# Kernel tuning notes

Hardware: AMD Instinct MI355X
Metric: run time of the kernel (lower is better)

The kernel has to match this reference:

```python
import jax, jax.numpy as jnp
import numpy as np
import math

VOCAB, D, H, L = 32000, 1024, 16, 4
HD = D // H
DFF = 4 * D
EPS = 1e-5


def setup_inputs() -> dict:
    key = jax.random.key(0)
    ks = jax.random.split(key, 20)
    B, T = 4, 1024
    s = 0.02
    inp = {
        'inputs': jax.random.randint(ks[0], (B, T), 0, VOCAB),
        'emb_table': jax.random.normal(ks[1], (VOCAB, D), jnp.float32) * s,
        'Wq': jax.random.normal(ks[2], (L, D, D), jnp.float32) * s,
        'bq': jnp.zeros((L, D), jnp.float32),
        'Wk': jax.random.normal(ks[3], (L, D, D), jnp.float32) * s,
        'bk': jnp.zeros((L, D), jnp.float32),
        'Wv': jax.random.normal(ks[4], (L, D, D), jnp.float32) * s,
        'bv': jnp.zeros((L, D), jnp.float32),
        'Wo': jax.random.normal(ks[5], (L, D, D), jnp.float32) * s,
        'bo': jnp.zeros((L, D), jnp.float32),
        'ln1_g': jnp.ones((L, D), jnp.float32),
        'ln1_b': jnp.zeros((L, D), jnp.float32),
        'W1': jax.random.normal(ks[6], (L, D, DFF), jnp.float32) * s,
        'b1': jnp.zeros((L, DFF), jnp.float32),
        'W2': jax.random.normal(ks[7], (L, DFF, D), jnp.float32) * s,
        'b2': jnp.zeros((L, D), jnp.float32),
        'ln2_g': jnp.ones((L, D), jnp.float32),
        'ln2_b': jnp.zeros((L, D), jnp.float32),
    }
    return inp


def _layernorm(x, g, b):
    mu = jnp.mean(x, axis=-1, keepdims=True)
    var = jnp.mean(jnp.square(x - mu), axis=-1, keepdims=True)
    return (x - mu) * jax.lax.rsqrt(var + EPS) * g + b


def _pos_emb(T):
    pos = jnp.arange(T, dtype=jnp.float32)[:, None]          # [T,1]
    div = jnp.exp(jnp.arange(0, D, 2, dtype=jnp.float32) * (-math.log(10000.0) / D))
    pe = jnp.zeros((T, D), jnp.float32)
    pe = pe.at[:, 0::2].set(jnp.sin(pos * div))
    pe = pe.at[:, 1::2].set(jnp.cos(pos * div))
    return pe


def reference(inputs, emb_table, Wq, bq, Wk, bk, Wv, bv, Wo, bo,
              ln1_g, ln1_b, W1, b1, W2, b2, ln2_g, ln2_b):
    B, T = inputs.shape
    x = emb_table[inputs] + _pos_emb(T)[None, :, :]          # [B,T,D]
    causal = jnp.tril(jnp.ones((T, T), bool))                # [T,T]
    scale = 1.0 / math.sqrt(HD)
    for l in range(L):
        q = (x @ Wq[l] + bq[l]).reshape(B, T, H, HD)
        k = (x @ Wk[l] + bk[l]).reshape(B, T, H, HD)
        v = (x @ Wv[l] + bv[l]).reshape(B, T, H, HD)
        scores = jnp.einsum('bqhd,bkhd->bhqk', q, k) * scale
        scores = jnp.where(causal, scores, -jnp.inf)
        w = jax.nn.softmax(scores, axis=-1)
        attn = jnp.einsum('bhqk,bkhd->bqhd', w, v).reshape(B, T, D)
        attn = attn @ Wo[l] + bo[l]
        x = _layernorm(x + attn, ln1_g[l], ln1_b[l])
        ff = jax.nn.relu(x @ W1[l] + b1[l]) @ W2[l] + b2[l]
        x = _layernorm(x + ff, ln2_g[l], ln2_b[l])
    return x
```

## Files before the change

### kernel.cpp

```cpp
#include <hip/hip_runtime.h>

typedef __attribute__((ext_vector_type(8))) __bf16 bf16x8;
typedef __attribute__((ext_vector_type(4))) float f32x4;
typedef __attribute__((ext_vector_type(8))) unsigned short ushort8;

#define DMODEL 1024
#define SEQ 1024
#define NLAYER 4

__device__ __forceinline__ unsigned short f2bf(float f) {
  unsigned u = __float_as_uint(f);
  u += 0x7fffu + ((u >> 16) & 1u);
  return (unsigned short)(u >> 16);
}

__device__ __forceinline__ float bf2f(unsigned short u) {
  return __uint_as_float((unsigned)u << 16);
}

__device__ __forceinline__ void async_copy16(const void* gsrc, const void* lds_dst) {
  __builtin_amdgcn_global_load_lds(
      (__attribute__((address_space(1))) void*)(unsigned long long)(gsrc),
      (__attribute__((address_space(3))) void*)(unsigned int)(unsigned long long)(lds_dst),
      16, 0, 0);
}

__device__ __forceinline__ f32x4 mfma16(bf16x8 a, bf16x8 b, f32x4 c) {
  return __builtin_amdgcn_mfma_f32_16x16x32_bf16(a, b, c, 0, 0, 0);
}

__global__ __launch_bounds__(256) void preproc_kernel(
    const int* __restrict__ tok, const float* __restrict__ emb,
    const float* __restrict__ Wq, const float* __restrict__ Wk,
    const float* __restrict__ Wv, const float* __restrict__ Wo,
    const float* __restrict__ W1, const float* __restrict__ W2,
    const float* __restrict__ bq, const float* __restrict__ bk,
    const float* __restrict__ bv,
    unsigned short* __restrict__ wqkv_t, unsigned short* __restrict__ wo_t,
    unsigned short* __restrict__ w1_t, unsigned short* __restrict__ w2_t,
    float* __restrict__ qkvb, unsigned short* __restrict__ xb) {
  __shared__ unsigned short tileT[64 * 136];
  const int bid = blockIdx.x;
  const int tid = threadIdx.x;
  if (bid < 6144) {
    const float* src; unsigned short* dst; size_t R, C; int tx, ty;
    if (bid < 2048) {
      int w = bid >> 9, z = (bid >> 7) & 3, tl = bid & 127;
      tx = tl & 15; ty = tl >> 4; R = 1024; C = 1024;
      if (w == 0)      { src = Wq + (size_t)z * 1048576; dst = wqkv_t + (size_t)z * 3145728; }
      else if (w == 1) { src = Wk + (size_t)z * 1048576; dst = wqkv_t + (size_t)z * 3145728 + 1048576; }
      else if (w == 2) { src = Wv + (size_t)z * 1048576; dst = wqkv_t + (size_t)z * 3145728 + 2097152; }
      else             { src = Wo + (size_t)z * 1048576; dst = wo_t + (size_t)z * 1048576; }
    } else if (bid < 4096) {
      int t = bid - 2048, z = t >> 9, tl = t & 511;
      tx = tl & 63; ty = tl >> 6; R = 1024; C = 4096;
      src = W1 + (size_t)z * 4194304; dst = w1_t + (size_t)z * 4194304;
    } else {
      int t = bid - 4096, z = t >> 9, tl = t & 511;
      tx = tl & 15; ty = tl >> 4; R = 4096; C = 1024;
      src = W2 + (size_t)z * 4194304; dst = w2_t + (size_t)z * 4194304;
    }
    const int c0 = tx * 64, r0 = ty * 128;
    const int s16 = tid & 15, hi = tid >> 4;
#pragma unroll
    for (int it = 0; it < 8; ++it) {
      const int r = it * 16 + hi;
      f32x4 v = __builtin_nontemporal_load(
          (const f32x4*)(src + (size_t)(r0 + r) * C + c0 + s16 * 4));
#pragma unroll
      for (int j = 0; j < 4; ++j) {
        const int c = s16 * 4 + j;
        tileT[c * 136 + (r ^ ((c & 7) << 3))] = f2bf(v[j]);
      }
    }
    __syncthreads();
#pragma unroll
    for (int p = 0; p < 4; ++p) {
      const int c = p * 16 + hi;
      ushort8 o = *(const ushort8*)&tileT[c * 136 + 8 * (s16 ^ (c & 7))];
      *(ushort8*)(dst + (size_t)(c0 + c) * R + r0 + s16 * 8) = o;
    }
  } else if (bid < 10240) {
    const int row = bid - 6144;
    const int t = row & (SEQ - 1);
    const int tk = tok[row];
    const int col = tid * 4;
    float4 e = *(const float4*)(emb + (size_t)tk * DMODEL + col);
    const float c = -9.21034037197618f / (float)DMODEL;
    float d0 = __expf((float)(col)*c);
    float d1 = __expf((float)(col + 2) * c);
    float a0 = (float)t * d0, a1 = (float)t * d1;
    e.x += sinf(a0); e.y += cosf(a0); e.z += sinf(a1); e.w += cosf(a1);
    ushort4 ub;
    ub.x = f2bf(e.x); ub.y = f2bf(e.y); ub.z = f2bf(e.z); ub.w = f2bf(e.w);
    *(ushort4*)(xb + (size_t)row * DMODEL + col) = ub;
  } else {
    int i = (bid - 10240) * 256 + tid;
    if (i < NLAYER * 3072) {
      int l = i / 3072, j = i % 3072;
      float v = (j < 1024) ? bq[l * 1024 + j]
              : (j < 2048) ? bk[l * 1024 + j - 1024]
                           : bv[l * 1024 + j - 2048];
      qkvb[i] = v;
    }
  }
}

#define G256_PHASE(BUF, MH, NH, STAGE_STMT, VM)                                   \
  {                                                                               \
    if (NH == 0) {                                                                \
      _Pragma("unroll") for (int fm = 0; fm < 4; ++fm)                            \
      _Pragma("unroll") for (int kk = 0; kk < 2; ++kk) {                          \
        int row = wr * 64 + fm * 16 + lr;                                         \
        int cb = (kk * 64 + g * 16) ^ ((row & 4) ? 32 : 0) ^ ((row & 8) ? 64 : 0);\
        af[fm][kk] = *(const bf16x8*)((const char*)&As[BUF][MH][0] + row * 128 + cb); \
      }                                                                           \
    }                                                                             \
    _Pragma("unroll") for (int fn = 0; fn < 2; ++fn)                              \
    _Pragma("unroll") for (int kk = 0; kk < 2; ++kk) {                            \
      int row = wc * 32 + fn * 16 + lr;                                           \
      int cb = (kk * 64 + g * 16) ^ ((row & 4) ? 32 : 0) ^ ((row & 8) ? 64 : 0);  \
      bfr[fn][kk] = *(const bf16x8*)((const char*)&Bs[BUF][NH][0] + row * 128 + cb); \
    }                                                                             \
    STAGE_STMT;                                                                   \
    if (VM == 1) asm volatile("s_waitcnt vmcnt(4)" ::: "memory");                 \
    if (VM == 2) asm volatile("s_waitcnt vmcnt(0)" ::: "memory");                 \
    asm volatile("s_barrier" ::: "memory");                                       \
    asm volatile("s_waitcnt lgkmcnt(0)" ::: "memory");                            \
    __builtin_amdgcn_s_setprio(1);                                                \
    _Pragma("unroll") for (int fm = 0; fm < 4; ++fm)                              \
    _Pragma("unroll") for (int fn = 0; fn < 2; ++fn)                              \
    _Pragma("unroll") for (int kk = 0; kk < 2; ++kk)                              \
      acc[MH][fm][NH][fn] = mfma16(af[fm][kk], bfr[fn][kk], acc[MH][fm][NH][fn]); \
    __builtin_amdgcn_s_setprio(0);                                                \
    asm volatile("s_barrier" ::: "memory");                                       \
  }

template <int QKV>
__global__ __launch_bounds__(512, 1) void gemm256(
    const unsigned short* __restrict__ A, const unsigned short* __restrict__ Bt,
    const float* __restrict__ bias, unsigned short* __restrict__ Cb,
    unsigned short* __restrict__ Cb2, int N) {
  __shared__ __align__(16) unsigned short As[2][2][8192];
  __shared__ __align__(16) unsigned short Bs[2][2][8192];
  constexpr int NK = 16;
  constexpr int NI = 8;

  const int tid = threadIdx.x;
  const int wid = tid >> 6, l = tid & 63;
  const int lr = l & 15, g = l >> 4;
  const int wr = wid >> 2, wc = wid & 3;

  const int gx = gridDim.x, nwg = gx * gridDim.y;
  int bid = blockIdx.y * gx + blockIdx.x;
  const int cpx = nwg >> 3;
  bid = (bid & 7) * cpx + (bid >> 3);
  const int rm = (bid / gx) * 256, rn = (bid % gx) * 256;

  const int kOff = ((l & 7) * 8) ^ ((l & 32) ? 16 : 0) ^ ((wid & 1) ? 32 : 0);
  const int rOff = wid * 8 + (l >> 3);

  auto stA = [&](int buf, int half, int t) {
#pragma unroll
    for (int r2 = 0; r2 < 2; ++r2) {
      const unsigned short* gs =
          A + (size_t)(rm + half * 128 + r2 * 64 + rOff) * 1024 + t * 64 + kOff;
      async_copy16(gs, &As[buf][half][r2 * 4096 + wid * 512]);
    }
  };
  auto stB = [&](int buf, int half, int t) {
#pragma unroll
    for (int r2 = 0; r2 < 2; ++r2) {
      const unsigned short* gs =
          Bt + (size_t)(rn + half * 128 + r2 * 64 + rOff) * 1024 + t * 64 + kOff;
      async_copy16(gs, &Bs[buf][half][r2 * 4096 + wid * 512]);
    }
  };

  f32x4 acc[2][4][2][2] = {};
  bf16x8 af[4][2], bfr[2][2];

  stA(0, 0, 0); stA(0, 1, 0); stB(0, 0, 0); stB(0, 1, 0);
  stA(1, 0, 1); stB(1, 0, 1);
  asm volatile("s_waitcnt vmcnt(4)" ::: "memory");
  asm volatile("s_barrier" ::: "memory");

  for (int i = 0; i < NI - 1; ++i) {
    const int t1 = 2 * i + 1, t2 = 2 * i + 2, t3 = 2 * i + 3;
    G256_PHASE(0, 0, 0, { stA(1, 1, t1); }, 0)
    G256_PHASE(0, 0, 1, { stB(1, 1, t1); }, 0)
    G256_PHASE(0, 1, 0, { stA(0, 0, t2); }, 0)
    G256_PHASE(0, 1, 1, { stB(0, 0, t2); }, 1)
    G256_PHASE(1, 0, 0, { stA(0, 1, t2); }, 0)
    G256_PHASE(1, 0, 1, { stB(0, 1, t2); }, 0)
    G256_PHASE(1, 1, 0, { if (t3 < NK) stA(1, 0, t3); }, 0)
    G256_PHASE(1, 1, 1, { if (t3 < NK) stB(1, 0, t3); }, 1)
  }
  {
    const int t1 = NK - 1;
    G256_PHASE(0, 0, 0, { stA(1, 1, t1); }, 0)
    G256_PHASE(0, 0, 1, { stB(1, 1, t1); }, 0)
    G256_PHASE(0, 1, 0, {}, 0)
    G256_PHASE(0, 1, 1, {}, 2)
    G256_PHASE(1, 0, 0, {}, 0)
    G256_PHASE(1, 0, 1, {}, 0)
    G256_PHASE(1, 1, 0, {}, 0)
    G256_PHASE(1, 1, 1, {}, 0)
  }

#pragma unroll
  for (int mh = 0; mh < 2; ++mh)
#pragma unroll
    for (int nh = 0; nh < 2; ++nh)
#pragma unroll
      for (int fn = 0; fn < 2; ++fn) {
        const int col = rn + nh * 128 + wc * 32 + fn * 16 + lr;
        const float bv = bias[col];
        if (QKV && col >= 2048) {
#pragma unroll
          for (int fm = 0; fm < 4; ++fm) {
            const int row0 = rm + mh * 128 + wr * 64 + fm * 16 + g * 4;
            ushort4 vv;
            vv.x = f2bf(acc[mh][fm][nh][fn][0] + bv);
            vv.y = f2bf(acc[mh][fm][nh][fn][1] + bv);
            vv.z = f2bf(acc[mh][fm][nh][fn][2] + bv);
            vv.w = f2bf(acc[mh][fm][nh][fn][3] + bv);
            *(ushort4*)(Cb2 + (size_t)(col - 2048) * 4096 + row0) = vv;
          }
        } else {
          const float sc = (QKV && col < 1024) ? 0.18033688011112042f : 1.0f;
          const int ldc = QKV ? 2048 : N;
#pragma unroll
          for (int fm = 0; fm < 4; ++fm)
#pragma unroll
            for (int r = 0; r < 4; ++r) {
              const int row = rm + mh * 128 + wr * 64 + fm * 16 + g * 4 + r;
              float v = (acc[mh][fm][nh][fn][r] + bv) * sc;
              if (!QKV) v = fmaxf(v, 0.0f);
              Cb[(size_t)row * ldc + col] = f2bf(v);
            }
        }
      }
}

__global__ __launch_bounds__(512, 2) void gemm_bf16w(
    const unsigned short* __restrict__ A, const unsigned short* __restrict__ Bt,
    const float* __restrict__ bias, unsigned short* __restrict__ Cb,
    const unsigned short* __restrict__ Xres, int N, int K) {
  __shared__ __align__(16) unsigned short As[2][8192];
  __shared__ __align__(16) unsigned short Bs[2][8192];
  const int tid = threadIdx.x;
  const int wid = tid >> 6, l = tid & 63, lr = l & 15, g = l >> 4;
  const int wr = wid >> 2, wc = wid & 3;
  const int d = blockIdx.y * 8 + blockIdx.x;
  const int xcd = d & 7, slot = d >> 3;
  const int bandsPerXcd = gridDim.y >> 3;
  const int by = xcd * bandsPerXcd + (slot >> 3);
  const int bx = slot & 7;
  const int rm = by * 128, rn = bx * 128;
  const int nk = K >> 6;

  const int kOff = ((l & 7) * 8) ^ ((l & 32) ? 16 : 0) ^ ((wid & 1) ? 32 : 0);
  const int rOff = wid * 8 + (l >> 3);

  auto stage = [&](int buf, int t) {
#pragma unroll
    for (int r2 = 0; r2 < 2; ++r2) {
      const unsigned short* ga =
          A + (size_t)(rm + r2 * 64 + rOff) * K + t * 64 + kOff;
      async_copy16(ga, &As[buf][r2 * 4096 + wid * 512]);
      const unsigned short* gb =
          Bt + (size_t)(rn + r2 * 64 + rOff) * K + t * 64 + kOff;
      async_copy16(gb, &Bs[buf][r2 * 4096 + wid * 512]);
    }
  };

  f32x4 acc[4][2] = {};
  stage(0, 0);
  asm volatile("s_waitcnt vmcnt(0)" ::: "memory");
  asm volatile("s_barrier" ::: "memory");

  for (int t = 0; t < nk; ++t) {
    const int cur = t & 1;
    if (t + 1 < nk) stage(cur ^ 1, t + 1);
    bf16x8 af[4][2], bfr[2][2];
#pragma unroll
    for (int fm = 0; fm < 4; ++fm)
#pragma unroll
      for (int kk = 0; kk < 2; ++kk) {
        int row = wr * 64 + fm * 16 + lr;
        int cb = (kk * 64 + g * 16) ^ ((row & 4) ? 32 : 0) ^ ((row & 8) ? 64 : 0);
        af[fm][kk] = *(const bf16x8*)((const char*)&As[cur][0] + row * 128 + cb);
      }
#pragma unroll
    for (int fn = 0; fn < 2; ++fn)
#pragma unroll
      for (int kk = 0; kk < 2; ++kk) {
        int row = wc * 32 + fn * 16 + lr;
        int cb = (kk * 64 + g * 16) ^ ((row & 4) ? 32 : 0) ^ ((row & 8) ? 64 : 0);
        bfr[fn][kk] = *(const bf16x8*)((const char*)&Bs[cur][0] + row * 128 + cb);
      }
    asm volatile("s_waitcnt lgkmcnt(0)" ::: "memory");
    __builtin_amdgcn_sched_barrier(0);
    __builtin_amdgcn_s_setprio(1);
#pragma unroll
    for (int fm = 0; fm < 4; ++fm)
#pragma unroll
      for (int fn = 0; fn < 2; ++fn)
#pragma unroll
        for (int kk = 0; kk < 2; ++kk)
          acc[fm][fn] = mfma16(af[fm][kk], bfr[fn][kk], acc[fm][fn]);
    __builtin_amdgcn_s_setprio(0);
    asm volatile("s_waitcnt vmcnt(0)" ::: "memory");
    asm volatile("s_barrier" ::: "memory");
  }

  const int row0 = rm + wr * 64 + g * 4;
  const int col0 = rn + wc * 32 + lr;
#pragma unroll
  for (int fn = 0; fn < 2; ++fn) {
    const int col = col0 + fn * 16;
    const float bv = bias[col];
#pragma unroll
    for (int fm = 0; fm < 4; ++fm)
#pragma unroll
      for (int r = 0; r < 4; ++r) {
        const int row = row0 + fm * 16 + r;
        float v = acc[fm][fn][r] + bv + bf2f(Xres[(size_t)row * N + col]);
        Cb[(size_t)row * N + col] = f2bf(v);
      }
  }
}

__global__ __launch_bounds__(256) void attn_kernel(
    const unsigned short* __restrict__ qk, const unsigned short* __restrict__ Vt,
    unsigned short* __restrict__ out) {
  __shared__ __align__(16) unsigned short Ks[2][64 * 64];
  __shared__ __align__(16) unsigned short Vs[2][64 * 64];
  __shared__ unsigned short Pl[4][32 * 72];
  const int tid = threadIdx.x;
  const int w = tid >> 6, l = tid & 63, lr = l & 15, g = l >> 4;
  const int bh = blockIdx.x;
  const int b = bh >> 4, h = bh & 15;
  const int byy = blockIdx.y;
  const int qblk = (byy < 4) ? (7 - byy) : (byy - 4);
  const int qb0 = qblk * 128 + w * 32;
  const size_t rowBase = (size_t)b * SEQ;
  const int cq = h * 64, ck = 1024 + h * 64;
  const int NTb = 2 * qblk + 2;

  const int sOff = ((l & 7) * 8) ^ ((l & 32) ? 16 : 0);
  const int sRow = l >> 3;

  auto stageKV = [&](int buf, int t) {
#pragma unroll
    for (int j = 0; j < 2; ++j) {
      const int row = w * 16 + j * 8 + sRow;
      const int off = sOff ^ (j ? 32 : 0);
      const unsigned short* gk =
          qk + (rowBase + t * 64 + row) * 2048 + ck + off;
      async_copy16(gk, &Ks[buf][(w * 16 + j * 8) * 64]);
      const unsigned short* gv =
          Vt + (size_t)(h * 64 + row) * 4096 + b * 1024 + t * 64 + off;
      async_copy16(gv, &Vs[buf][(w * 16 + j * 8) * 64]);
    }
  };

  bf16x8 aq[2][2];
#pragma unroll
  for (int qf = 0; qf < 2; ++qf)
#pragma unroll
    for (int ks = 0; ks < 2; ++ks)
      aq[qf][ks] = *(const bf16x8*)(qk + (rowBase + qb0 + qf * 16 + lr) * 2048 +
                                    cq + ks * 32 + g * 8);

  f32x4 o[2][4] = {};
  float l_[2][4] = {};

  const int rdswz = ((lr & 4) ? 16 : 0) ^ ((lr & 8) ? 32 : 0);

  stageKV(0, 0);
  asm volatile("s_waitcnt vmcnt(0)" ::: "memory");
  asm volatile("s_barrier" ::: "memory");

  for (int kt = 0; kt < NTb; ++kt) {
    const int k0 = kt * 64;
    const int cur = kt & 1;
    if (kt + 1 < NTb) stageKV(cur ^ 1, kt + 1);
    bf16x8 kf[4][2];
#pragma unroll
    for (int kg = 0; kg < 4; ++kg)
#pragma unroll
      for (int ks = 0; ks < 2; ++ks)
        kf[kg][ks] = *(const bf16x8*)&Ks[cur][(kg * 16 + lr) * 64 +
                                             ((ks * 32 + g * 8) ^ rdswz)];
    f32x4 s[2][4] = {};
#pragma unroll
    for (int kg = 0; kg < 4; ++kg)
#pragma unroll
      for (int qf = 0; qf < 2; ++qf) {
        s[qf][kg] = mfma16(aq[qf][0], kf[kg][0], s[qf][kg]);
        s[qf][kg] = mfma16(aq[qf][1], kf[kg][1], s[qf][kg]);
      }
    if (k0 + 63 <= qb0) {
#pragma unroll
      for (int qf = 0; qf < 2; ++qf)
#pragma unroll
        for (int r = 0; r < 4; ++r) {
          float e0 = exp2f(s[qf][0][r]);
          float e1 = exp2f(s[qf][1][r]);
          float e2 = exp2f(s[qf][2][r]);
          float e3 = exp2f(s[qf][3][r]);
          l_[qf][r] += (e0 + e1) + (e2 + e3);
          unsigned short* pr = &Pl[w][(qf * 16 + g * 4 + r) * 72];
          pr[lr] = f2bf(e0);
          pr[16 + lr] = f2bf(e1);
          pr[32 + lr] = f2bf(e2);
          pr[48 + lr] = f2bf(e3);
        }
    } else {
#pragma unroll
      for (int qf = 0; qf < 2; ++qf)
#pragma unroll
        for (int r = 0; r < 4; ++r) {
          const int q = qb0 + qf * 16 + g * 4 + r;
          float e0 = (k0 + lr <= q) ? exp2f(s[qf][0][r]) : 0.0f;
          float e1 = (k0 + 16 + lr <= q) ? exp2f(s[qf][1][r]) : 0.0f;
          float e2 = (k0 + 32 + lr <= q) ? exp2f(s[qf][2][r]) : 0.0f;
          float e3 = (k0 + 48 + lr <= q) ? exp2f(s[qf][3][r]) : 0.0f;
          l_[qf][r] += (e0 + e1) + (e2 + e3);
          unsigned short* pr = &Pl[w][(qf * 16 + g * 4 + r) * 72];
          pr[lr] = f2bf(e0);
          pr[16 + lr] = f2bf(e1);
          pr[32 + lr] = f2bf(e2);
          pr[48 + lr] = f2bf(e3);
        }
    }
    asm volatile("s_waitcnt lgkmcnt(0)" ::: "memory");
    __builtin_amdgcn_sched_barrier(0);
    bf16x8 pa[2][2];
#pragma unroll
    for (int qf = 0; qf < 2; ++qf)
#pragma unroll
      for (int kc = 0; kc < 2; ++kc)
        pa[qf][kc] = *(const bf16x8*)&Pl[w][(qf * 16 + lr) * 72 + kc * 32 + g * 8];
    bf16x8 vf[4][2];
#pragma unroll
    for (int nbv = 0; nbv < 4; ++nbv)
#pragma unroll
      for (int ks = 0; ks < 2; ++ks)
        vf[nbv][ks] = *(const bf16x8*)&Vs[cur][(nbv * 16 + lr) * 64 +
                                               ((ks * 32 + g * 8) ^ rdswz)];
#pragma unroll
    for (int nbv = 0; nbv < 4; ++nbv)
#pragma unroll
      for (int qf = 0; qf < 2; ++qf) {
        o[qf][nbv] = mfma16(pa[qf][0], vf[nbv][0], o[qf][nbv]);
        o[qf][nbv] = mfma16(pa[qf][1], vf[nbv][1], o[qf][nbv]);
      }
    asm volatile("s_waitcnt vmcnt(0)" ::: "memory");
    asm volatile("s_barrier" ::: "memory");
  }
  float rinv[2][4];
#pragma unroll
  for (int qf = 0; qf < 2; ++qf)
#pragma unroll
    for (int r = 0; r < 4; ++r) {
      float t = l_[qf][r];
      t += __shfl_xor(t, 1, 64);
      t += __shfl_xor(t, 2, 64);
      t += __shfl_xor(t, 4, 64);
      t += __shfl_xor(t, 8, 64);
      rinv[qf][r] = __builtin_amdgcn_rcpf(t);
    }
#pragma unroll
  for (int qf = 0; qf < 2; ++qf)
#pragma unroll
    for (int nbv = 0; nbv < 4; ++nbv)
#pragma unroll
      for (int r = 0; r < 4; ++r) {
        float val = o[qf][nbv][r] * rinv[qf][r];
        out[(rowBase + qb0 + qf * 16 + g * 4 + r) * 1024 + h * 64 + nbv * 16 + lr] =
            f2bf(val);
      }
}

__global__ __launch_bounds__(256) void ln_kernel(
    const unsigned short* __restrict__ tin,
    const float* __restrict__ gam, const float* __restrict__ bet,
    unsigned short* __restrict__ xbf, float* __restrict__ out2) {
  const int w = threadIdx.x >> 6, lane = threadIdx.x & 63;
  const int row = blockIdx.x * 4 + w;
  const size_t base = (size_t)row * DMODEL;
  const int c0 = lane * 8;
  const int c1 = 512 + lane * 8;
  ushort8 u0 = *(const ushort8*)(tin + base + c0);
  ushort8 u1 = *(const ushort8*)(tin + base + c1);
  float v[16];
#pragma unroll
  for (int i = 0; i < 8; ++i) { v[i] = bf2f(u0[i]); v[8 + i] = bf2f(u1[i]); }
  float s = 0.0f, ss = 0.0f;
#pragma unroll
  for (int i = 0; i < 16; ++i) { s += v[i]; ss += v[i] * v[i]; }
#pragma unroll
  for (int msk = 32; msk; msk >>= 1) {
    s += __shfl_xor(s, msk, 64);
    ss += __shfl_xor(ss, msk, 64);
  }
  const float mean = s * (1.0f / DMODEL);
  const float var = ss * (1.0f / DMODEL) - mean * mean;
  const float inv = rsqrtf(var + 1e-5f);
  float gv[16], bv[16];
  *(float4*)(gv + 0) = *(const float4*)(gam + c0);
  *(float4*)(gv + 4) = *(const float4*)(gam + c0 + 4);
  *(float4*)(gv + 8) = *(const float4*)(gam + c1);
  *(float4*)(gv + 12) = *(const float4*)(gam + c1 + 4);
  *(float4*)(bv + 0) = *(const float4*)(bet + c0);
  *(float4*)(bv + 4) = *(const float4*)(bet + c0 + 4);
  *(float4*)(bv + 8) = *(const float4*)(bet + c1);
  *(float4*)(bv + 12) = *(const float4*)(bet + c1 + 4);
  float ov[16];
#pragma unroll
  for (int i = 0; i < 16; ++i) ov[i] = (v[i] - mean) * inv * gv[i] + bv[i];
  ushort8 o0, o1;
#pragma unroll
  for (int i = 0; i < 8; ++i) { o0[i] = f2bf(ov[i]); o1[i] = f2bf(ov[8 + i]); }
  *(ushort8*)(xbf + base + c0) = o0;
  *(ushort8*)(xbf + base + c1) = o1;
  if (out2) {
    *(float4*)(out2 + base + c0) = *(float4*)(ov + 0);
    *(float4*)(out2 + base + c0 + 4) = *(float4*)(ov + 4);
    *(float4*)(out2 + base + c1) = *(float4*)(ov + 8);
    *(float4*)(out2 + base + c1 + 4) = *(float4*)(ov + 12);
  }
}

extern "C" void kernel_launch(void* const* d_in, const int* in_sizes, int n_in,
                              void* d_out, int out_size, void* d_ws, size_t ws_size,
                              hipStream_t stream) {
  (void)in_sizes; (void)n_in; (void)out_size; (void)ws_size;
  const int* tok = (const int*)d_in[0];
  const float* emb = (const float*)d_in[1];
  const float* Wq = (const float*)d_in[2];
  const float* bq = (const float*)d_in[3];
  const float* Wk = (const float*)d_in[4];
  const float* bk = (const float*)d_in[5];
  const float* Wv = (const float*)d_in[6];
  const float* bv = (const float*)d_in[7];
  const float* Wo = (const float*)d_in[8];
  const float* bo = (const float*)d_in[9];
  const float* ln1g = (const float*)d_in[10];
  const float* ln1b = (const float*)d_in[11];
  const float* W1 = (const float*)d_in[12];
  const float* b1 = (const float*)d_in[13];
  const float* W2 = (const float*)d_in[14];
  const float* b2 = (const float*)d_in[15];
  const float* ln2g = (const float*)d_in[16];
  const float* ln2b = (const float*)d_in[17];

  char* ws = (char*)d_ws;
  size_t off = 0;
  auto alloc = [&](size_t bytes) {
    char* p = ws + off;
    off += (bytes + 255) & ~(size_t)255;
    return p;
  };
  unsigned short* wqkv_t = (unsigned short*)alloc((size_t)NLAYER * 3072 * 1024 * 2);
  unsigned short* wo_t = (unsigned short*)alloc((size_t)NLAYER * 1024 * 1024 * 2);
  unsigned short* w1_t = (unsigned short*)alloc((size_t)NLAYER * 4096 * 1024 * 2);
  unsigned short* w2_t = (unsigned short*)alloc((size_t)NLAYER * 1024 * 4096 * 2);
  float* qkvb = (float*)alloc((size_t)NLAYER * 3072 * 4);
  unsigned short* yb = (unsigned short*)alloc((size_t)4096 * 1024 * 2);
  unsigned short* xb = (unsigned short*)alloc((size_t)4096 * 1024 * 2);
  unsigned short* qkbuf = (unsigned short*)alloc((size_t)4096 * 2048 * 2);
  unsigned short* vt = (unsigned short*)alloc((size_t)1024 * 4096 * 2);
  unsigned short* attn = (unsigned short*)alloc((size_t)4096 * 1024 * 2);
  unsigned short* hb = (unsigned short*)alloc((size_t)4096 * 4096 * 2);

  preproc_kernel<<<dim3(10288), dim3(256), 0, stream>>>(
      tok, emb, Wq, Wk, Wv, Wo, W1, W2, bq, bk, bv,
      wqkv_t, wo_t, w1_t, w2_t, qkvb, xb);

  for (int l = 0; l < NLAYER; ++l) {
    gemm256<1><<<dim3(12, 16), dim3(512), 0, stream>>>(
        xb, wqkv_t + (size_t)l * 3145728, qkvb + l * 3072, qkbuf, vt, 3072);
    attn_kernel<<<dim3(64, 8), dim3(256), 0, stream>>>(qkbuf, vt, attn);
    gemm_bf16w<<<dim3(8, 32), dim3(512), 0, stream>>>(
        attn, wo_t + (size_t)l * 1048576, bo + l * 1024, yb, xb, 1024, 1024);
    ln_kernel<<<dim3(1024), dim3(256), 0, stream>>>(
        yb, ln1g + l * 1024, ln1b + l * 1024, xb, nullptr);
    gemm256<0><<<dim3(16, 16), dim3(512), 0, stream>>>(
        xb, w1_t + (size_t)l * 4194304, b1 + l * 4096, hb, nullptr, 4096);
    gemm_bf16w<<<dim3(8, 32), dim3(512), 0, stream>>>(
        hb, w2_t + (size_t)l * 4194304, b2 + l * 1024, yb, xb, 1024, 4096);
    ln_kernel<<<dim3(1024), dim3(256), 0, stream>>>(
        yb, ln2g + l * 1024, ln2b + l * 1024, xb,
        (l == NLAYER - 1) ? (float*)d_out : nullptr);
  }
}
```

Measured before the change: 797.4 us.

## Triple-buffer residual GEMM with split A/B staging and two-phase MFMA

Converts the residual-add GEMM from double to triple buffering in LDS, prefetching two k-tiles ahead. A and B tile loads are issued separately and interleaved with two half-steps of MFMA work, each with its own barrier. Partial vmcnt waits keep loads in flight across iterations. LDS use rises to 96KB and launch bounds drop to one block per CU, trading occupancy for deeper prefetch and more barriers.

```diff
diff --git a/kernel.cpp b/kernel.cpp
--- a/kernel.cpp
+++ b/kernel.cpp
@@ -243,12 +243,12 @@
       }
 }
 
-__global__ __launch_bounds__(512, 2) void gemm_bf16w(
+__global__ __launch_bounds__(512, 1) void gemm_bf16w(
     const unsigned short* __restrict__ A, const unsigned short* __restrict__ Bt,
     const float* __restrict__ bias, unsigned short* __restrict__ Cb,
     const unsigned short* __restrict__ Xres, int N, int K) {
-  __shared__ __align__(16) unsigned short As[2][8192];
-  __shared__ __align__(16) unsigned short Bs[2][8192];
+  __shared__ __align__(16) unsigned short As[3][8192];
+  __shared__ __align__(16) unsigned short Bs[3][8192];
   const int tid = threadIdx.x;
   const int wid = tid >> 6, l = tid & 63, lr = l & 15, g = l >> 4;
   const int wr = wid >> 2, wc = wid & 3;
@@ -263,12 +263,17 @@
   const int kOff = ((l & 7) * 8) ^ ((l & 32) ? 16 : 0) ^ ((wid & 1) ? 32 : 0);
   const int rOff = wid * 8 + (l >> 3);
 
-  auto stage = [&](int buf, int t) {
+  auto stA = [&](int buf, int t) {
 #pragma unroll
     for (int r2 = 0; r2 < 2; ++r2) {
       const unsigned short* ga =
           A + (size_t)(rm + r2 * 64 + rOff) * K + t * 64 + kOff;
       async_copy16(ga, &As[buf][r2 * 4096 + wid * 512]);
+    }
+  };
+  auto stB = [&](int buf, int t) {
+#pragma unroll
+    for (int r2 = 0; r2 < 2; ++r2) {
       const unsigned short* gb =
           Bt + (size_t)(rn + r2 * 64 + rOff) * K + t * 64 + kOff;
       async_copy16(gb, &Bs[buf][r2 * 4096 + wid * 512]);
@@ -276,16 +281,17 @@
   };
 
   f32x4 acc[4][2] = {};
-  stage(0, 0);
-  asm volatile("s_waitcnt vmcnt(0)" ::: "memory");
+  bf16x8 af[4][2], bfr[2][2];
+
+  stA(0, 0); stB(0, 0);
+  stA(1, 1); stB(1, 1);
+  asm volatile("s_waitcnt vmcnt(4)" ::: "memory");
   asm volatile("s_barrier" ::: "memory");
 
   for (int t = 0; t < nk; ++t) {
-    const int cur = t & 1;
-    if (t + 1 < nk) stage(cur ^ 1, t + 1);
-    bf16x8 af[4][2], bfr[2][2];
-#pragma unroll
-    for (int fm = 0; fm < 4; ++fm)
+    const int cur = t % 3;
+#pragma unroll
+    for (int fm = 0; fm < 2; ++fm)
 #pragma unroll
       for (int kk = 0; kk < 2; ++kk) {
         int row = wr * 64 + fm * 16 + lr;
@@ -300,18 +306,46 @@
         int cb = (kk * 64 + g * 16) ^ ((row & 4) ? 32 : 0) ^ ((row & 8) ? 64 : 0);
         bfr[fn][kk] = *(const bf16x8*)((const char*)&Bs[cur][0] + row * 128 + cb);
       }
+    if (t + 2 < nk) stA((t + 2) % 3, t + 2);
+    asm volatile("s_barrier" ::: "memory");
     asm volatile("s_waitcnt lgkmcnt(0)" ::: "memory");
     __builtin_amdgcn_sched_barrier(0);
     __builtin_amdgcn_s_setprio(1);
 #pragma unroll
-    for (int fm = 0; fm < 4; ++fm)
+    for (int fm = 0; fm < 2; ++fm)
 #pragma unroll
       for (int fn = 0; fn < 2; ++fn)
 #pragma unroll
         for (int kk = 0; kk < 2; ++kk)
           acc[fm][fn] = mfma16(af[fm][kk], bfr[fn][kk], acc[fm][fn]);
     __builtin_amdgcn_s_setprio(0);
-    asm volatile("s_waitcnt vmcnt(0)" ::: "memory");
+    asm volatile("s_barrier" ::: "memory");
+#pragma unroll
+    for (int fm = 2; fm < 4; ++fm)
+#pragma unroll
+      for (int kk = 0; kk < 2; ++kk) {
+        int row = wr * 64 + fm * 16 + lr;
+        int cb = (kk * 64 + g * 16) ^ ((row & 4) ? 32 : 0) ^ ((row & 8) ? 64 : 0);
+        af[fm][kk] = *(const bf16x8*)((const char*)&As[cur][0] + row * 128 + cb);
+      }
+    if (t + 2 < nk) {
+      stB((t + 2) % 3, t + 2);
+      asm volatile("s_waitcnt vmcnt(4)" ::: "memory");
+    } else if (t + 1 < nk) {
+      asm volatile("s_waitcnt vmcnt(0)" ::: "memory");
+    }
+    asm volatile("s_barrier" ::: "memory");
+    asm volatile("s_waitcnt lgkmcnt(0)" ::: "memory");
+    __builtin_amdgcn_sched_barrier(0);
+    __builtin_amdgcn_s_setprio(1);
+#pragma unroll
+    for (int fm = 2; fm < 4; ++fm)
+#pragma unroll
+      for (int fn = 0; fn < 2; ++fn)
+#pragma unroll
+        for (int kk = 0; kk < 2; ++kk)
+          acc[fm][fn] = mfma16(af[fm][kk], bfr[fn][kk], acc[fm][fn]);
+    __builtin_amdgcn_s_setprio(0);
     asm volatile("s_barrier" ::: "memory");
   }
 
```

Result: no change. 809.8 us (+1.6%).
